# Optimization experiments

Measured on AMD Instinct MI355X. Metric: run time of the kernel, lower is better.

Reference implementation:

```python
import jax, jax.numpy as jnp
import numpy as np

B, C, D = 512, 1000, 512
K = 10


def setup_inputs() -> dict:
    key = jax.random.key(0)
    k1, k2, k3, k4, k5 = jax.random.split(key, 5)
    x = jax.random.normal(k1, (B, D), dtype=jnp.float32)
    protos = jax.random.normal(k2, (C, D), dtype=jnp.float32)
    # ex2/ex1 chosen so N*ex2^2 - ex1^2 > 0 (valid sqrt)
    ex2 = jax.random.uniform(k3, (C, D), dtype=jnp.float32) + 1.0
    ex1 = jax.random.uniform(k4, (C, D), dtype=jnp.float32) * 0.1
    cls_num = jax.random.randint(k5, (C,), 1, 100, dtype=jnp.int32)
    proto_label = jnp.arange(C, dtype=jnp.int32)
    return {"x": x, "protos": protos, "ex2": ex2, "ex1": ex1,
            "cls_num": cls_num, "proto_label": proto_label, "k_nearest": K}


def reference(x, protos, ex2, ex1, cls_num, proto_label, k_nearest):
    # rd: per-class, per-feature variance proxy  [C, D]
    N = cls_num[:, None].astype(ex2.dtype)
    rd = jnp.sqrt(N * ex2 ** 2 - ex1 ** 2)
    # softmax over feature dim of (rowmax - rd)
    rd = jax.nn.softmax(jnp.max(rd, axis=1, keepdims=True) - rd, axis=1)
    # weighted squared distances: [B, C, D] -> reduce D -> [B, C]
    diff = x[:, None, :] - protos[None, :, :]
    x_dists = diff ** 2 * rd[None, :, :]
    simi_mat = x_dists.sum(axis=2)  # [B, C]
    # k smallest distances (torch.topk largest=False)
    neg_vals, topk_index = jax.lax.top_k(-simi_mat, k_nearest)
    topk_vals = -neg_vals  # [B, K]
    topk_conf = topk_vals.sum(axis=1, keepdims=True) / topk_vals  # [B, K]
    # pick prototype with max confidence, map through label table
    temp = jnp.argmax(topk_conf, axis=1)  # [B]
    ans_index = jnp.take_along_axis(topk_index, temp[:, None], axis=1)[:, 0]
    predict = proto_label[ans_index]  # [B]
    return predict, topk_conf
```

## Files before the change

kernel.cpp:

```cpp
#include <hip/hip_runtime.h>
#include <math.h>
#include <float.h>

#define B_SZ 512
#define C_SZ 1000
#define D_SZ 512
#define K_TOP 10
#define K2 1024
#define NSPLIT 8
#define KSPLIT (K2 / NSPLIT)
#define BC (B_SZ * C_SZ)

#define W_OFF   0
#define T3_OFF  (W_OFF + C_SZ * K2)
#define PART_OFF (T3_OFF + 1024)

__global__ __launch_bounds__(256) void prep_kernel(const float* __restrict__ protos,
                                                   const float* __restrict__ ex2,
                                                   const float* __restrict__ ex1,
                                                   const int* __restrict__ cls_num,
                                                   float* __restrict__ ws) {
    float* W  = ws + W_OFF;
    float* t3 = ws + T3_OFF;
    const int wid  = threadIdx.x >> 6;
    const int lane = threadIdx.x & 63;
    const int c = blockIdx.x * 4 + wid;

    const size_t rb = (size_t)c * D_SZ + lane * 8;
    float e2v[8], e1v[8], pv[8];
    *(float4*)&e2v[0] = *(const float4*)(ex2 + rb);
    *(float4*)&e2v[4] = *(const float4*)(ex2 + rb + 4);
    *(float4*)&e1v[0] = *(const float4*)(ex1 + rb);
    *(float4*)&e1v[4] = *(const float4*)(ex1 + rb + 4);
    *(float4*)&pv[0]  = *(const float4*)(protos + rb);
    *(float4*)&pv[4]  = *(const float4*)(protos + rb + 4);
    const float N = (float)cls_num[c];

    float v[8], mn = FLT_MAX;
    #pragma unroll
    for (int k = 0; k < 8; k++) {
        v[k] = sqrtf(N * e2v[k] * e2v[k] - e1v[k] * e1v[k]);
        mn = fminf(mn, v[k]);
    }
    #pragma unroll
    for (int off = 1; off < 64; off <<= 1) mn = fminf(mn, __shfl_xor(mn, off));

    float ev[8], s = 0.f;
    #pragma unroll
    for (int k = 0; k < 8; k++) { ev[k] = expf(mn - v[k]); s += ev[k]; }
    #pragma unroll
    for (int off = 1; off < 64; off <<= 1) s += __shfl_xor(s, off);
    const float inv = 1.0f / s;

    float w1[8], w2[8], t = 0.f;
    #pragma unroll
    for (int k = 0; k < 8; k++) {
        const float rdv = ev[k] * inv;
        w1[k] = rdv;
        w2[k] = -2.0f * rdv * pv[k];
        t = fmaf(rdv * pv[k], pv[k], t);
    }
    float* wr = W + (size_t)c * K2 + lane * 8;
    *(float4*)(wr)            = *(float4*)&w1[0];
    *(float4*)(wr + 4)        = *(float4*)&w1[4];
    *(float4*)(wr + D_SZ)     = *(float4*)&w2[0];
    *(float4*)(wr + D_SZ + 4) = *(float4*)&w2[4];
    #pragma unroll
    for (int off = 1; off < 64; off <<= 1) t += __shfl_xor(t, off);
    if (lane == 0) t3[c] = t;
}

#define TM 64
#define TN 64
#define KB 32

__global__ __launch_bounds__(256, 4) void gemm_kernel(const float* __restrict__ x,
                                                      const float* __restrict__ Wm,
                                                      float* __restrict__ part) {
    __shared__ float as[KB][TM + 4];
    __shared__ float wsm[KB][TN + 4];

    const int tid = threadIdx.x;
    const int tx = tid & 15;
    const int ty = tid >> 4;
    const int c0 = blockIdx.x * TN;
    const int b0 = blockIdx.y * TM;
    const int kz = blockIdx.z;

    const int row0 = tid >> 3;
    const int row1 = row0 + 32;
    const int col4 = (tid & 7) * 4;

    const bool sq = (kz < NSPLIT / 2);
    const int khalf0 = sq ? kz * KSPLIT : kz * KSPLIT - D_SZ;

    float acc[4][4] = {};

    for (int ch = 0; ch < KSPLIT / KB; ch++) {
        const int kx = khalf0 + ch * KB;
        const int kw = kz * KSPLIT + ch * KB;

        float4 a0 = *(const float4*)(x + (size_t)(b0 + row0) * D_SZ + kx + col4);
        float4 a1 = *(const float4*)(x + (size_t)(b0 + row1) * D_SZ + kx + col4);
        if (sq) {
            a0.x *= a0.x; a0.y *= a0.y; a0.z *= a0.z; a0.w *= a0.w;
            a1.x *= a1.x; a1.y *= a1.y; a1.z *= a1.z; a1.w *= a1.w;
        }
        const int cc0 = c0 + row0, cc1 = c0 + row1;
        float4 w0 = make_float4(0.f, 0.f, 0.f, 0.f);
        float4 w1 = make_float4(0.f, 0.f, 0.f, 0.f);
        if (cc0 < C_SZ) w0 = *(const float4*)(Wm + (size_t)cc0 * K2 + kw + col4);
        if (cc1 < C_SZ) w1 = *(const float4*)(Wm + (size_t)cc1 * K2 + kw + col4);

        as[col4 + 0][row0] = a0.x; as[col4 + 1][row0] = a0.y;
        as[col4 + 2][row0] = a0.z; as[col4 + 3][row0] = a0.w;
        as[col4 + 0][row1] = a1.x; as[col4 + 1][row1] = a1.y;
        as[col4 + 2][row1] = a1.z; as[col4 + 3][row1] = a1.w;
        wsm[col4 + 0][row0] = w0.x; wsm[col4 + 1][row0] = w0.y;
        wsm[col4 + 2][row0] = w0.z; wsm[col4 + 3][row0] = w0.w;
        wsm[col4 + 0][row1] = w1.x; wsm[col4 + 1][row1] = w1.y;
        wsm[col4 + 2][row1] = w1.z; wsm[col4 + 3][row1] = w1.w;
        __syncthreads();

        #pragma unroll
        for (int kk = 0; kk < KB; kk++) {
            const float4 av4 = *(const float4*)&as[kk][ty * 4];
            const float4 wv4 = *(const float4*)&wsm[kk][tx * 4];
            const float a[4] = {av4.x, av4.y, av4.z, av4.w};
            const float w[4] = {wv4.x, wv4.y, wv4.z, wv4.w};
            #pragma unroll
            for (int i = 0; i < 4; i++)
                #pragma unroll
                for (int j = 0; j < 4; j++)
                    acc[i][j] = fmaf(a[i], w[j], acc[i][j]);
        }
        __syncthreads();
    }

    float* o = part + (size_t)kz * BC;
    #pragma unroll
    for (int i = 0; i < 4; i++) {
        const int b = b0 + ty * 4 + i;
        const int c = c0 + tx * 4;
        if (c + 3 < C_SZ) {
            float4 v = {acc[i][0], acc[i][1], acc[i][2], acc[i][3]};
            *(float4*)(o + (size_t)b * C_SZ + c) = v;
        } else {
            #pragma unroll
            for (int j = 0; j < 4; j++)
                if (c + j < C_SZ) o[(size_t)b * C_SZ + c + j] = acc[i][j];
        }
    }
}

__global__ __launch_bounds__(256) void topk_kernel(const float* __restrict__ ws,
                                                   const int* __restrict__ proto_label,
                                                   float* __restrict__ out) {
    const float* part = ws + PART_OFF;
    const float* t3   = ws + T3_OFF;
    const int wid = threadIdx.x >> 6;
    const int lane = threadIdx.x & 63;
    const int b = blockIdx.x * 4 + wid;

    float vals[16];
    #pragma unroll
    for (int j = 0; j < 16; j++) {
        const int c = lane + j * 64;
        if (c < C_SZ) {
            const size_t idx = (size_t)b * C_SZ + c;
            float s = t3[c];
            #pragma unroll
            for (int z = 0; z < NSPLIT; z++)
                s += part[(size_t)z * BC + idx];
            vals[j] = s;
        } else {
            vals[j] = FLT_MAX;
        }
    }

    float kv[K_TOP];
    int ki[K_TOP];
    for (int t = 0; t < K_TOP; t++) {
        float bv = FLT_MAX;
        int bi = 0x7fffffff;
        #pragma unroll
        for (int j = 0; j < 16; j++) {
            const int c = lane + j * 64;
            if (vals[j] < bv) { bv = vals[j]; bi = c; }
        }
        #pragma unroll
        for (int off = 1; off < 64; off <<= 1) {
            const float ov = __shfl_xor(bv, off);
            const int oi = __shfl_xor(bi, off);
            if (ov < bv || (ov == bv && oi < bi)) { bv = ov; bi = oi; }
        }
        kv[t] = bv;
        ki[t] = bi;
        if ((bi & 63) == lane) vals[bi >> 6] = FLT_MAX;
    }

    if (lane == 0) {
        float S = 0.f;
        #pragma unroll
        for (int t = 0; t < K_TOP; t++) S += kv[t];
        float conf[K_TOP];
        #pragma unroll
        for (int t = 0; t < K_TOP; t++) {
            conf[t] = S / kv[t];
            out[B_SZ + b * K_TOP + t] = conf[t];
        }
        int best = 0;
        for (int t = 1; t < K_TOP; t++)
            if (conf[t] > conf[best]) best = t;
        out[b] = (float)proto_label[ki[best]];
    }
}

extern "C" void kernel_launch(void* const* d_in, const int* in_sizes, int n_in,
                              void* d_out, int out_size, void* d_ws, size_t ws_size,
                              hipStream_t stream) {
    const float* x           = (const float*)d_in[0];
    const float* protos      = (const float*)d_in[1];
    const float* ex2         = (const float*)d_in[2];
    const float* ex1         = (const float*)d_in[3];
    const int*   cls_num     = (const int*)d_in[4];
    const int*   proto_label = (const int*)d_in[5];

    float* ws  = (float*)d_ws;
    float* out = (float*)d_out;

    prep_kernel<<<C_SZ / 4, 256, 0, stream>>>(protos, ex2, ex1, cls_num, ws);

    dim3 g2((C_SZ + TN - 1) / TN, B_SZ / TM, NSPLIT);
    gemm_kernel<<<g2, 256, 0, stream>>>(x, ws + W_OFF, ws + PART_OFF);

    topk_kernel<<<B_SZ / 4, 256, 0, stream>>>(ws, proto_label, out);
}
```

Baseline: 106.1 us.

## Emulate FP32 GEMM with split-FP16 MFMA and halve K-split count

```diff
diff --git a/kernel.cpp b/kernel.cpp
--- a/kernel.cpp
+++ b/kernel.cpp
@@ -7,20 +7,30 @@
 #define D_SZ 512
 #define K_TOP 10
 #define K2 1024
-#define NSPLIT 8
+#define NSPLIT 4
 #define KSPLIT (K2 / NSPLIT)
 #define BC (B_SZ * C_SZ)
 
-#define W_OFF   0
-#define T3_OFF  (W_OFF + C_SZ * K2)
+#define WHI_OFF 0
+#define WLO_OFF (C_SZ * K2)
+#define T3_OFF  (C_SZ * K2)
 #define PART_OFF (T3_OFF + 1024)
+
+using f16x8 = __attribute__((ext_vector_type(8))) _Float16;
+using f32x4 = __attribute__((ext_vector_type(4))) float;
+
+__device__ __forceinline__ void split2(float v, _Float16& h, _Float16& l) {
+    h = (_Float16)v;
+    l = (_Float16)(v - (float)h);
+}
 
 __global__ __launch_bounds__(256) void prep_kernel(const float* __restrict__ protos,
                                                    const float* __restrict__ ex2,
                                                    const float* __restrict__ ex1,
                                                    const int* __restrict__ cls_num,
                                                    float* __restrict__ ws) {
-    float* W  = ws + W_OFF;
+    _Float16* Whi = (_Float16*)ws + WHI_OFF;
+    _Float16* Wlo = (_Float16*)ws + WLO_OFF;
     float* t3 = ws + T3_OFF;
     const int wid  = threadIdx.x >> 6;
     const int lane = threadIdx.x & 63;
@@ -52,103 +62,136 @@
     for (int off = 1; off < 64; off <<= 1) s += __shfl_xor(s, off);
     const float inv = 1.0f / s;
 
-    float w1[8], w2[8], t = 0.f;
+    f16x8 h1, l1, h2, l2;
+    float t = 0.f;
     #pragma unroll
     for (int k = 0; k < 8; k++) {
         const float rdv = ev[k] * inv;
-        w1[k] = rdv;
-        w2[k] = -2.0f * rdv * pv[k];
+        const float w2  = -2.0f * rdv * pv[k];
+        _Float16 hh, ll;
+        split2(rdv, hh, ll); h1[k] = hh; l1[k] = ll;
+        split2(w2,  hh, ll); h2[k] = hh; l2[k] = ll;
         t = fmaf(rdv * pv[k], pv[k], t);
     }
-    float* wr = W + (size_t)c * K2 + lane * 8;
-    *(float4*)(wr)            = *(float4*)&w1[0];
-    *(float4*)(wr + 4)        = *(float4*)&w1[4];
-    *(float4*)(wr + D_SZ)     = *(float4*)&w2[0];
-    *(float4*)(wr + D_SZ + 4) = *(float4*)&w2[4];
+    _Float16* wh = Whi + (size_t)c * K2 + lane * 8;
+    _Float16* wl = Wlo + (size_t)c * K2 + lane * 8;
+    *(f16x8*)(wh)         = h1;
+    *(f16x8*)(wh + D_SZ)  = h2;
+    *(f16x8*)(wl)         = l1;
+    *(f16x8*)(wl + D_SZ)  = l2;
+
     #pragma unroll
     for (int off = 1; off < 64; off <<= 1) t += __shfl_xor(t, off);
     if (lane == 0) t3[c] = t;
 }
 
-#define TM 64
-#define TN 64
-#define KB 32
-
-__global__ __launch_bounds__(256, 4) void gemm_kernel(const float* __restrict__ x,
-                                                      const float* __restrict__ Wm,
+#define BM 64
+#define BN 64
+#define BK 32
+#define LDT 40
+
+__global__ __launch_bounds__(256, 2) void gemm_kernel(const float* __restrict__ x,
+                                                      const _Float16* __restrict__ Whi,
+                                                      const _Float16* __restrict__ Wlo,
                                                       float* __restrict__ part) {
-    __shared__ float as[KB][TM + 4];
-    __shared__ float wsm[KB][TN + 4];
-
-    const int tid = threadIdx.x;
-    const int tx = tid & 15;
-    const int ty = tid >> 4;
-    const int c0 = blockIdx.x * TN;
-    const int b0 = blockIdx.y * TM;
+    __shared__ __align__(16) _Float16 Ah[BM][LDT];
+    __shared__ __align__(16) _Float16 Al[BM][LDT];
+    __shared__ __align__(16) _Float16 Bh[BN][LDT];
+    __shared__ __align__(16) _Float16 Bl[BN][LDT];
+
+    const int tid  = threadIdx.x;
+    const int lane = tid & 63;
+    const int w    = tid >> 6;
+    const int c0 = blockIdx.x * BN;
+    const int b0 = blockIdx.y * BM;
     const int kz = blockIdx.z;
-
-    const int row0 = tid >> 3;
-    const int row1 = row0 + 32;
-    const int col4 = (tid & 7) * 4;
-
     const bool sq = (kz < NSPLIT / 2);
     const int khalf0 = sq ? kz * KSPLIT : kz * KSPLIT - D_SZ;
 
-    float acc[4][4] = {};
-
-    for (int ch = 0; ch < KSPLIT / KB; ch++) {
-        const int kx = khalf0 + ch * KB;
-        const int kw = kz * KSPLIT + ch * KB;
-
-        float4 a0 = *(const float4*)(x + (size_t)(b0 + row0) * D_SZ + kx + col4);
-        float4 a1 = *(const float4*)(x + (size_t)(b0 + row1) * D_SZ + kx + col4);
+    const int srow = tid >> 2;
+    const int sseg = (tid & 3) * 8;
+    const int mw = (w >> 1) * 32;
+    const int nw = (w & 1) * 32;
+    const int lr = lane & 15;
+    const int kg = lane >> 4;
+
+    f32x4 acc[2][2];
+    #pragma unroll
+    for (int i = 0; i < 2; i++)
+        #pragma unroll
+        for (int j = 0; j < 2; j++)
+            #pragma unroll
+            for (int r = 0; r < 4; r++) acc[i][j][r] = 0.f;
+
+    const int cW = c0 + srow;
+
+    for (int ch = 0; ch < KSPLIT / BK; ch++) {
+        const int kx = khalf0 + ch * BK + sseg;
+        const int kw = kz * KSPLIT + ch * BK + sseg;
+
+        float4 a0 = *(const float4*)(x + (size_t)(b0 + srow) * D_SZ + kx);
+        float4 a1 = *(const float4*)(x + (size_t)(b0 + srow) * D_SZ + kx + 4);
         if (sq) {
             a0.x *= a0.x; a0.y *= a0.y; a0.z *= a0.z; a0.w *= a0.w;
             a1.x *= a1.x; a1.y *= a1.y; a1.z *= a1.z; a1.w *= a1.w;
         }
-        const int cc0 = c0 + row0, cc1 = c0 + row1;
-        float4 w0 = make_float4(0.f, 0.f, 0.f, 0.f);
-        float4 w1 = make_float4(0.f, 0.f, 0.f, 0.f);
-        if (cc0 < C_SZ) w0 = *(const float4*)(Wm + (size_t)cc0 * K2 + kw + col4);
-        if (cc1 < C_SZ) w1 = *(const float4*)(Wm + (size_t)cc1 * K2 + kw + col4);
-
-        as[col4 + 0][row0] = a0.x; as[col4 + 1][row0] = a0.y;
-        as[col4 + 2][row0] = a0.z; as[col4 + 3][row0] = a0.w;
-        as[col4 + 0][row1] = a1.x; as[col4 + 1][row1] = a1.y;
-        as[col4 + 2][row1] = a1.z; as[col4 + 3][row1] = a1.w;
-        wsm[col4 + 0][row0] = w0.x; wsm[col4 + 1][row0] = w0.y;
-        wsm[col4 + 2][row0] = w0.z; wsm[col4 + 3][row0] = w0.w;
-        wsm[col4 + 0][row1] = w1.x; wsm[col4 + 1][row1] = w1.y;
-        wsm[col4 + 2][row1] = w1.z; wsm[col4 + 3][row1] = w1.w;
+        const float av[8] = {a0.x, a0.y, a0.z, a0.w, a1.x, a1.y, a1.z, a1.w};
+        f16x8 ah, al;
+        #pragma unroll
+        for (int j = 0; j < 8; j++) {
+            _Float16 hh, ll;
+            split2(av[j], hh, ll);
+            ah[j] = hh; al[j] = ll;
+        }
+
+        f16x8 wh, wl;
+        if (cW < C_SZ) {
+            wh = *(const f16x8*)(Whi + (size_t)cW * K2 + kw);
+            wl = *(const f16x8*)(Wlo + (size_t)cW * K2 + kw);
+        } else {
+            #pragma unroll
+            for (int j = 0; j < 8; j++) { wh[j] = (_Float16)0.f; wl[j] = (_Float16)0.f; }
+        }
+
         __syncthreads();
-
-        #pragma unroll
-        for (int kk = 0; kk < KB; kk++) {
-            const float4 av4 = *(const float4*)&as[kk][ty * 4];
-            const float4 wv4 = *(const float4*)&wsm[kk][tx * 4];
-            const float a[4] = {av4.x, av4.y, av4.z, av4.w};
-            const float w[4] = {wv4.x, wv4.y, wv4.z, wv4.w};
-            #pragma unroll
-            for (int i = 0; i < 4; i++)
+        *(f16x8*)&Ah[srow][sseg] = ah;
+        *(f16x8*)&Al[srow][sseg] = al;
+        *(f16x8*)&Bh[srow][sseg] = wh;
+        *(f16x8*)&Bl[srow][sseg] = wl;
+        __syncthreads();
+
+        f16x8 fah[2], fal[2], fbh[2], fbl[2];
+        #pragma unroll
+        for (int i = 0; i < 2; i++) {
+            fah[i] = *(const f16x8*)&Ah[mw + i * 16 + lr][kg * 8];
+            fal[i] = *(const f16x8*)&Al[mw + i * 16 + lr][kg * 8];
+            fbh[i] = *(const f16x8*)&Bh[nw + i * 16 + lr][kg * 8];
+            fbl[i] = *(const f16x8*)&Bl[nw + i * 16 + lr][kg * 8];
+        }
+        #pragma unroll
+        for (int i = 0; i < 2; i++)
+            #pragma unroll
+            for (int j = 0; j < 2; j++) {
+                acc[i][j] = __builtin_amdgcn_mfma_f32_16x16x32_f16(fal[i], fbl[j], acc[i][j], 0, 0, 0);
+                acc[i][j] = __builtin_amdgcn_mfma_f32_16x16x32_f16(fah[i], fbl[j], acc[i][j], 0, 0, 0);
+                acc[i][j] = __builtin_amdgcn_mfma_f32_16x16x32_f16(fal[i], fbh[j], acc[i][j], 0, 0, 0);
+                acc[i][j] = __builtin_amdgcn_mfma_f32_16x16x32_f16(fah[i], fbh[j], acc[i][j], 0, 0, 0);
+            }
+    }
+
+    float* o = part + (size_t)kz * BC;
+    #pragma unroll
+    for (int i = 0; i < 2; i++) {
+        #pragma unroll
+        for (int j = 0; j < 2; j++) {
+            const int c = c0 + nw + j * 16 + lr;
+            if (c < C_SZ) {
                 #pragma unroll
-                for (int j = 0; j < 4; j++)
-                    acc[i][j] = fmaf(a[i], w[j], acc[i][j]);
-        }
-        __syncthreads();
-    }
-
-    float* o = part + (size_t)kz * BC;
-    #pragma unroll
-    for (int i = 0; i < 4; i++) {
-        const int b = b0 + ty * 4 + i;
-        const int c = c0 + tx * 4;
-        if (c + 3 < C_SZ) {
-            float4 v = {acc[i][0], acc[i][1], acc[i][2], acc[i][3]};
-            *(float4*)(o + (size_t)b * C_SZ + c) = v;
-        } else {
-            #pragma unroll
-            for (int j = 0; j < 4; j++)
-                if (c + j < C_SZ) o[(size_t)b * C_SZ + c + j] = acc[i][j];
+                for (int r = 0; r < 4; r++) {
+                    const int b = b0 + mw + i * 16 + kg * 4 + r;
+                    o[(size_t)b * C_SZ + c] = acc[i][j][r];
+                }
+            }
         }
     }
 }
@@ -231,8 +274,11 @@
 
     prep_kernel<<<C_SZ / 4, 256, 0, stream>>>(protos, ex2, ex1, cls_num, ws);
 
-    dim3 g2((C_SZ + TN - 1) / TN, B_SZ / TM, NSPLIT);
-    gemm_kernel<<<g2, 256, 0, stream>>>(x, ws + W_OFF, ws + PART_OFF);
+    dim3 g2((C_SZ + BN - 1) / BN, B_SZ / BM, NSPLIT);
+    gemm_kernel<<<g2, 256, 0, stream>>>(x,
+                                        (const _Float16*)ws + WHI_OFF,
+                                        (const _Float16*)ws + WLO_OFF,
+                                        ws + PART_OFF);
 
     topk_kernel<<<B_SZ / 4, 256, 0, stream>>>(ws, proto_label, out);
 }
```

New measurement: 93.67 us. 1.13x faster.
